# Kernel tuning notes

Hardware: AMD Instinct MI355X
Metric: run time of the kernel (lower is better)

The kernel has to match this reference:

```python
import jax, jax.numpy as jnp
import numpy as np

C, N, KS = 64, 64, 3  # channels, spatial size, kernel size (matches init_kwargs)
B = 4


def identity_kernel(c, k):
    # 'full' identity kernel: delta at spatial center on the channel diagonal
    ker = np.zeros((c, c, k, k), np.float32)
    ker[np.arange(c), np.arange(c), k // 2, k // 2] = 1.0
    return jnp.asarray(ker)


def setup_inputs() -> dict:
    key = jax.random.key(0)
    k1, k2, k3 = jax.random.split(key, 3)
    conv_in = jax.random.normal(k1, (B, C, N, N), jnp.float32)
    # small kernel perturbation, as produced by a hypernetwork at near-init ('I + net')
    K = jax.random.normal(k2, (B, C, C, KS, KS), jnp.float32) * 0.05
    bias = jax.random.normal(k3, (B, C, 1, 1), jnp.float32)
    return {"conv_in": conv_in, "K": K, "bias": bias}


def _circ_conv_one(x, ker):
    # x: [c, n, n], ker: [co, ci, kh, kw]; circular-padded cross-correlation (torch conv2d semantics)
    p = KS // 2
    xp = jnp.pad(x, ((0, 0), (p, p), (p, p)), mode="wrap")
    out = jax.lax.conv_general_dilated(
        xp[None], ker, window_strides=(1, 1), padding="VALID",
        dimension_numbers=("NCHW", "OIHW", "NCHW"))
    return out[0]  # [c, n, n]


def reference(conv_in, K, bias):
    # kernel_init == 'I + net': add identity kernel
    Kfull = K + identity_kernel(C, KS)[None]  # [B, c, c, k, k]

    # batch spatial circular conv2D with per-sample kernels
    conv_out = jax.vmap(_circ_conv_one)(conv_in, Kfull) + bias  # [B, c, n, n]

    # spectral log-determinant of the circular conv operator:
    # embed kernel into n x n grid, FFT2 over space, then per-frequency c x c logdet.
    # (per-frequency phase factors from kernel centering have unit modulus, so
    #  log|det| is independent of the spatial alignment convention)
    Kpad = jnp.zeros((K.shape[0], C, C, N, N), K.dtype).at[..., :KS, :KS].set(Kfull)
    Khat = jnp.fft.fft2(Kpad)                    # [B, c, c, n, n] complex
    Khat = jnp.moveaxis(Khat, (1, 2), (3, 4))    # [B, n, n, c, c]
    _, logabsdet = jnp.linalg.slogdet(Khat)      # [B, n, n]
    logdet = jnp.sum(logabsdet, axis=(1, 2))     # [B]

    return conv_out, logdet
```

## Files before the change

### kernel.cpp

```cpp
#include <hip/hip_runtime.h>
#include <hip/hip_fp16.h>
#include <math.h>

#define TAU 0.5f

__device__ __forceinline__ int h2i(__half2 h) { int i; __builtin_memcpy(&i, &h, 4); return i; }
__device__ __forceinline__ __half2 i2h(int i) { __half2 h; __builtin_memcpy(&h, &i, 4); return h; }

__global__ __launch_bounds__(256, 3) void fused_kernel(
    const float* __restrict__ x, const float* __restrict__ K,
    const float* __restrict__ bias, float* __restrict__ out,
    float* __restrict__ logdet) {
  __shared__ float smem[4736];
  int bid = blockIdx.x;
  int t = threadIdx.x;

  bool isConv = false;
  int cid = 0, lid = 0;
  if (bid < 2304) {
    int q9 = bid / 9, m9 = bid - q9 * 9;
    if (m9 == 8) { isConv = true; cid = q9; }
    else lid = bid - (bid + 1) / 9;
  } else {
    lid = bid - 256;
  }

  if (isConv) {
    int b = cid >> 6, co = cid & 63;
    float* w = smem;
    float* tile = smem + 576;

    for (int i = t; i < 576; i += 256) {
      float vv = K[(size_t)((b * 64 + co) * 64) * 9 + i];
      if (i == co * 9 + 4) vv += 1.0f;
      w[i] = vv;
    }

    int ty = t >> 2;
    int tx = t & 3;
    int x0 = tx << 4;
    float bval = bias[b * 64 + co];
    float acc[16];
#pragma unroll
    for (int i = 0; i < 16; ++i) acc[i] = bval;

    const float* xb = x + (size_t)(b * 64) * 4096;
    for (int ci = 0; ci < 64; ++ci) {
      __syncthreads();
      const float* xc = xb + (size_t)ci * 4096;
#pragma unroll
      for (int j = 0; j < 16; ++j) {
        int i = t + 256 * j;
        tile[(i >> 6) * 65 + (i & 63)] = xc[i];
      }
      __syncthreads();

      float w0 = w[ci * 9 + 0], w1 = w[ci * 9 + 1], w2 = w[ci * 9 + 2];
      float w3 = w[ci * 9 + 3], w4 = w[ci * 9 + 4], w5 = w[ci * 9 + 5];
      float w6 = w[ci * 9 + 6], w7 = w[ci * 9 + 7], w8 = w[ci * 9 + 8];

      int ym = ((ty - 1) & 63) * 65;
      int yc = ty * 65;
      int yp = ((ty + 1) & 63) * 65;
      float in0[18], in1[18], in2[18];
#pragma unroll
      for (int ix = 0; ix < 18; ++ix) {
        int xx = (x0 + ix - 1) & 63;
        in0[ix] = tile[ym + xx];
        in1[ix] = tile[yc + xx];
        in2[ix] = tile[yp + xx];
      }
#pragma unroll
      for (int px = 0; px < 16; ++px) {
        float a = acc[px];
        a = fmaf(w0, in0[px], a); a = fmaf(w1, in0[px + 1], a); a = fmaf(w2, in0[px + 2], a);
        a = fmaf(w3, in1[px], a); a = fmaf(w4, in1[px + 1], a); a = fmaf(w5, in1[px + 2], a);
        a = fmaf(w6, in2[px], a); a = fmaf(w7, in2[px + 1], a); a = fmaf(w8, in2[px + 2], a);
        acc[px] = a;
      }
    }

    float* op = out + (size_t)(b * 64 + co) * 4096 + ty * 64 + x0;
#pragma unroll
    for (int i = 0; i < 16; i += 4) {
      *(float4*)(op + i) = make_float4(acc[i], acc[i + 1], acc[i + 2], acc[i + 3]);
    }
    return;
  }

  int u, v;
  if (lid < 33) { u = 0; v = lid; }
  else if (lid < 2017) { int q = lid - 33; u = 1 + (q >> 6); v = q & 63; }
  else { u = 32; v = lid - 2017; }
  float weight = (((u & 31) == 0) && ((v & 31) == 0)) ? 1.0f : 2.0f;

  int b = t >> 6;
  int r = t & 63;

  float Ar[3], Ai[3], Br[3], Bi[3];
  {
    const float k2pi = -6.283185307179586f / 64.0f;
    float su, cu, sv, cv;
    __sincosf(k2pi * (float)u, &su, &cu);
    __sincosf(k2pi * (float)v, &sv, &cv);
    Ar[0] = 1.0f; Ai[0] = 0.0f; Ar[1] = cu; Ai[1] = su;
    Ar[2] = cu * cu - su * su; Ai[2] = 2.0f * cu * su;
    Br[0] = 1.0f; Bi[0] = 0.0f; Br[1] = cv; Bi[1] = sv;
    Br[2] = cv * cv - sv * sv; Bi[2] = 2.0f * cv * sv;
  }
  float wr[9], wi[9];
#pragma unroll
  for (int kh = 0; kh < 3; ++kh)
#pragma unroll
    for (int kw = 0; kw < 3; ++kw) {
      wr[kh * 3 + kw] = Ar[kh] * Br[kw] - Ai[kh] * Bi[kw];
      wi[kh * 3 + kw] = Ar[kh] * Bi[kw] + Ai[kh] * Br[kw];
    }

  __half2 a2[65];
  const float4* Kp4 = (const float4*)(K + (size_t)(b * 64 + r) * 576);
#pragma unroll
  for (int g = 0; g < 16; ++g) {
    float f[36];
#pragma unroll
    for (int qq = 0; qq < 9; ++qq) {
      float4 vv = Kp4[g * 9 + qq];
      f[qq * 4 + 0] = vv.x; f[qq * 4 + 1] = vv.y; f[qq * 4 + 2] = vv.z; f[qq * 4 + 3] = vv.w;
    }
#pragma unroll
    for (int cc = 0; cc < 4; ++cc) {
      int c = g * 4 + cc;
      float re = 0.0f, im = 0.0f;
#pragma unroll
      for (int t9 = 0; t9 < 9; ++t9) {
        float kv = f[cc * 9 + t9];
        re = fmaf(kv, wr[t9], re);
        im = fmaf(kv, wi[t9], im);
      }
      if (c == r) { re += wr[4]; im += wi[4]; }
      a2[c] = __floats2half2_rn(re, im);
    }
  }
  a2[64] = __floats2half2_rn(0.0f, 0.0f);

  bool active = true;
  float pivmag = 1.0f;

  for (int k = 0; k < 63; ++k) {
    float fr0 = __low2float(a2[0]);
    float fi0 = __high2float(a2[0]);
    float mag = fmaf(fr0, fr0, fi0 * fi0);
    bool cand = active && (mag >= TAU);
    unsigned long long candm = __ballot(cand);
    int p;
    if (candm != 0ULL) {
      p = __ffsll(candm) - 1;
    } else {
      float mm = active ? mag : -1.0f;
#pragma unroll
      for (int off = 32; off > 0; off >>= 1) mm = fmaxf(mm, __shfl_xor(mm, off));
      unsigned long long mx = __ballot(active && (mag == mm));
      if (mx == 0ULL) mx = __ballot(active);
      p = __ffsll(mx) - 1;
    }
    p &= 63;

    bool isPiv = (r == p);
    pivmag = isPiv ? mag : pivmag;
    active = active && !isPiv;

    __half2 pivh = i2h(__builtin_amdgcn_readlane(h2i(a2[0]), p));
    float pr = __low2float(pivh);
    float pi = __high2float(pivh);
    float inv = __builtin_amdgcn_rcpf(fmaf(pr, pr, pi * pi));
    float fre = (fr0 * pr + fi0 * pi) * inv;
    float fim = (fi0 * pr - fr0 * pi) * inv;
    fre = active ? fre : 0.0f;
    fim = active ? fim : 0.0f;
    __half2 nfre2 = __float2half2_rn(-fre);
    __half2 fim2 = __halves2half2(__float2half_rn(fim),
                                  __float2half_rn(-fim));

    int rem = 63 - k;
#pragma unroll
    for (int ch = 0; ch < 8; ++ch) {
      if (ch * 8 < rem) {
        int c0 = ch * 8 + 1;
        int Li[8];
#pragma unroll
        for (int e = 0; e < 8; ++e)
          Li[e] = __builtin_amdgcn_readlane(h2i(a2[c0 + e]), p);
#pragma unroll
        for (int e = 0; e < 8; ++e) {
          __half2 P = i2h(Li[e]);
          __half2 tmp = __hfma2(nfre2, P, a2[c0 + e]);
          a2[c0 + e - 1] = __hfma2(fim2, __lowhigh2highlow(P), tmp);
        }
      }
    }
  }
  {
    float fr0 = __low2float(a2[0]);
    float fi0 = __high2float(a2[0]);
    if (active) pivmag = fmaf(fr0, fr0, fi0 * fi0);
  }

  float logsum = 0.5f * __logf(pivmag);
#pragma unroll
  for (int off = 32; off > 0; off >>= 1) logsum += __shfl_xor(logsum, off);
  if (r == 0) atomicAdd(&logdet[b], weight * logsum);
}

extern "C" void kernel_launch(void* const* d_in, const int* in_sizes, int n_in,
                              void* d_out, int out_size, void* d_ws, size_t ws_size,
                              hipStream_t stream) {
  const float* conv_in = (const float*)d_in[0];
  const float* K       = (const float*)d_in[1];
  const float* bias    = (const float*)d_in[2];
  float* out = (float*)d_out;
  float* logdet = out + 1048576;

  hipMemsetAsync(logdet, 0, 4 * sizeof(float), stream);
  fused_kernel<<<dim3(2306), dim3(256), 0, stream>>>(conv_in, K, bias, out, logdet);
}
```

Measured before the change: 336.9 us.

## Spill trailing matrix columns to LDS to raise occupancy of LU kernel

The per-lane complex LU factorization now keeps only the first 40 columns of each row in registers and stores the remaining 24 in shared memory, updated with LDS reads and writes. The launch-bound occupancy hint rises from 3 to 8 blocks, and the DFT twiddles are made wave-uniform via readfirstlane. The 3x3 conv inner loop is restructured row by row to cut live registers. The intent is higher occupancy to hide latency, at the cost of extra LDS traffic and a larger shared allocation per block.

After: 333.7 us. About the same (-0.9%).

```diff
diff --git a/kernel.cpp b/kernel.cpp
--- a/kernel.cpp
+++ b/kernel.cpp
@@ -4,14 +4,17 @@
 
 #define TAU 0.5f
 
+#define REGC 40
+#define LDSC 24
+
 __device__ __forceinline__ int h2i(__half2 h) { int i; __builtin_memcpy(&i, &h, 4); return i; }
 __device__ __forceinline__ __half2 i2h(int i) { __half2 h; __builtin_memcpy(&h, &i, 4); return h; }
 
-__global__ __launch_bounds__(256, 3) void fused_kernel(
+__global__ __launch_bounds__(256, 8) void fused_kernel(
     const float* __restrict__ x, const float* __restrict__ K,
     const float* __restrict__ bias, float* __restrict__ out,
     float* __restrict__ logdet) {
-  __shared__ float smem[4736];
+  __shared__ float smem[6144];
   int bid = blockIdx.x;
   int t = threadIdx.x;
 
@@ -55,28 +58,36 @@
       }
       __syncthreads();
 
-      float w0 = w[ci * 9 + 0], w1 = w[ci * 9 + 1], w2 = w[ci * 9 + 2];
-      float w3 = w[ci * 9 + 3], w4 = w[ci * 9 + 4], w5 = w[ci * 9 + 5];
-      float w6 = w[ci * 9 + 6], w7 = w[ci * 9 + 7], w8 = w[ci * 9 + 8];
-
       int ym = ((ty - 1) & 63) * 65;
       int yc = ty * 65;
       int yp = ((ty + 1) & 63) * 65;
-      float in0[18], in1[18], in2[18];
-#pragma unroll
-      for (int ix = 0; ix < 18; ++ix) {
-        int xx = (x0 + ix - 1) & 63;
-        in0[ix] = tile[ym + xx];
-        in1[ix] = tile[yc + xx];
-        in2[ix] = tile[yp + xx];
-      }
-#pragma unroll
-      for (int px = 0; px < 16; ++px) {
-        float a = acc[px];
-        a = fmaf(w0, in0[px], a); a = fmaf(w1, in0[px + 1], a); a = fmaf(w2, in0[px + 2], a);
-        a = fmaf(w3, in1[px], a); a = fmaf(w4, in1[px + 1], a); a = fmaf(w5, in1[px + 2], a);
-        a = fmaf(w6, in2[px], a); a = fmaf(w7, in2[px + 1], a); a = fmaf(w8, in2[px + 2], a);
-        acc[px] = a;
+
+      {
+        float wa = w[ci * 9 + 0], wb = w[ci * 9 + 1], wcc = w[ci * 9 + 2];
+        float in[18];
+#pragma unroll
+        for (int ix = 0; ix < 18; ++ix) in[ix] = tile[ym + ((x0 + ix - 1) & 63)];
+#pragma unroll
+        for (int px = 0; px < 16; ++px)
+          acc[px] = fmaf(wa, in[px], fmaf(wb, in[px + 1], fmaf(wcc, in[px + 2], acc[px])));
+      }
+      {
+        float wa = w[ci * 9 + 3], wb = w[ci * 9 + 4], wcc = w[ci * 9 + 5];
+        float in[18];
+#pragma unroll
+        for (int ix = 0; ix < 18; ++ix) in[ix] = tile[yc + ((x0 + ix - 1) & 63)];
+#pragma unroll
+        for (int px = 0; px < 16; ++px)
+          acc[px] = fmaf(wa, in[px], fmaf(wb, in[px + 1], fmaf(wcc, in[px + 2], acc[px])));
+      }
+      {
+        float wa = w[ci * 9 + 6], wb = w[ci * 9 + 7], wcc = w[ci * 9 + 8];
+        float in[18];
+#pragma unroll
+        for (int ix = 0; ix < 18; ++ix) in[ix] = tile[yp + ((x0 + ix - 1) & 63)];
+#pragma unroll
+        for (int px = 0; px < 16; ++px)
+          acc[px] = fmaf(wa, in[px], fmaf(wb, in[px + 1], fmaf(wcc, in[px + 2], acc[px])));
       }
     }
 
@@ -88,6 +99,7 @@
     return;
   }
 
+  int* sm32 = (int*)smem;
   int u, v;
   if (lid < 33) { u = 0; v = lid; }
   else if (lid < 2017) { int q = lid - 33; u = 1 + (q >> 6); v = q & 63; }
@@ -97,8 +109,9 @@
   int b = t >> 6;
   int r = t & 63;
 
-  float Ar[3], Ai[3], Br[3], Bi[3];
+  int swr[9], swi[9];
   {
+    float Ar[3], Ai[3], Br[3], Bi[3];
     const float k2pi = -6.283185307179586f / 64.0f;
     float su, cu, sv, cv;
     __sincosf(k2pi * (float)u, &su, &cu);
@@ -107,41 +120,34 @@
     Ar[2] = cu * cu - su * su; Ai[2] = 2.0f * cu * su;
     Br[0] = 1.0f; Bi[0] = 0.0f; Br[1] = cv; Bi[1] = sv;
     Br[2] = cv * cv - sv * sv; Bi[2] = 2.0f * cv * sv;
-  }
-  float wr[9], wi[9];
-#pragma unroll
-  for (int kh = 0; kh < 3; ++kh)
-#pragma unroll
-    for (int kw = 0; kw < 3; ++kw) {
-      wr[kh * 3 + kw] = Ar[kh] * Br[kw] - Ai[kh] * Bi[kw];
-      wi[kh * 3 + kw] = Ar[kh] * Bi[kw] + Ai[kh] * Br[kw];
-    }
-
-  __half2 a2[65];
-  const float4* Kp4 = (const float4*)(K + (size_t)(b * 64 + r) * 576);
-#pragma unroll
-  for (int g = 0; g < 16; ++g) {
-    float f[36];
-#pragma unroll
-    for (int qq = 0; qq < 9; ++qq) {
-      float4 vv = Kp4[g * 9 + qq];
-      f[qq * 4 + 0] = vv.x; f[qq * 4 + 1] = vv.y; f[qq * 4 + 2] = vv.z; f[qq * 4 + 3] = vv.w;
-    }
-#pragma unroll
-    for (int cc = 0; cc < 4; ++cc) {
-      int c = g * 4 + cc;
-      float re = 0.0f, im = 0.0f;
-#pragma unroll
-      for (int t9 = 0; t9 < 9; ++t9) {
-        float kv = f[cc * 9 + t9];
-        re = fmaf(kv, wr[t9], re);
-        im = fmaf(kv, wi[t9], im);
-      }
-      if (c == r) { re += wr[4]; im += wi[4]; }
-      a2[c] = __floats2half2_rn(re, im);
-    }
-  }
-  a2[64] = __floats2half2_rn(0.0f, 0.0f);
+#pragma unroll
+    for (int kh = 0; kh < 3; ++kh)
+#pragma unroll
+      for (int kw = 0; kw < 3; ++kw) {
+        float wrv = Ar[kh] * Br[kw] - Ai[kh] * Bi[kw];
+        float wiv = Ar[kh] * Bi[kw] + Ai[kh] * Br[kw];
+        swr[kh * 3 + kw] = __builtin_amdgcn_readfirstlane(__float_as_int(wrv));
+        swi[kh * 3 + kw] = __builtin_amdgcn_readfirstlane(__float_as_int(wiv));
+      }
+  }
+
+  __half2 a2[REGC + 1];
+  const float* Kp = K + (size_t)(b * 64 + r) * 576;
+#pragma unroll
+  for (int c = 0; c < 64; ++c) {
+    float re = 0.0f, im = 0.0f;
+#pragma unroll
+    for (int t9 = 0; t9 < 9; ++t9) {
+      float kv = Kp[c * 9 + t9];
+      re = fmaf(kv, __int_as_float(swr[t9]), re);
+      im = fmaf(kv, __int_as_float(swi[t9]), im);
+    }
+    if (c == r) { re += __int_as_float(swr[4]); im += __int_as_float(swi[4]); }
+    __half2 h = __floats2half2_rn(re, im);
+    if (c < REGC) a2[c] = h;
+    else sm32[(b * LDSC + (c - REGC)) * 64 + r] = h2i(h);
+  }
+  a2[REGC] = __floats2half2_rn(0.0f, 0.0f);
 
   bool active = true;
   float pivmag = 1.0f;
@@ -182,9 +188,10 @@
                                   __float2half_rn(-fim));
 
     int rem = 63 - k;
-#pragma unroll
-    for (int ch = 0; ch < 8; ++ch) {
-      if (ch * 8 < rem) {
+    int RR = rem < REGC ? rem : REGC;
+#pragma unroll
+    for (int ch = 0; ch < 5; ++ch) {
+      if (ch * 8 < RR) {
         int c0 = ch * 8 + 1;
         int Li[8];
 #pragma unroll
@@ -196,6 +203,26 @@
           __half2 tmp = __hfma2(nfre2, P, a2[c0 + e]);
           a2[c0 + e - 1] = __hfma2(fim2, __lowhigh2highlow(P), tmp);
         }
+      }
+    }
+
+    if (k < LDSC) {
+      int base = (b * LDSC + k) * 64;
+      int own = base + r;
+      int pva = base + p;
+      {
+        __half2 pv = i2h(sm32[pva]);
+        __half2 mine = i2h(sm32[own]);
+        __half2 tmp = __hfma2(nfre2, pv, mine);
+        a2[REGC - 1] = __hfma2(fim2, __lowhigh2highlow(pv), tmp);
+      }
+#pragma unroll 4
+      for (int cl = k + 1; cl < LDSC; ++cl) {
+        own += 64; pva += 64;
+        __half2 pv = i2h(sm32[pva]);
+        __half2 mine = i2h(sm32[own]);
+        __half2 tmp = __hfma2(nfre2, pv, mine);
+        sm32[own] = h2i(__hfma2(fim2, __lowhigh2highlow(pv), tmp));
       }
     }
   }
```
